# Kernel optimization log

Hardware: AMD Instinct MI355X
Metric: run time of the kernel (lower is better)

## Reference

```python
import jax, jax.numpy as jnp
import numpy as np

Z_DIM, Y_DIM, X_DIM, N_ACT = 32, 16, 64, 4
TINY_H, HEAD_H = 64, 32
INNER_STEPS, SUP_STEPS = 2, 2
BATCH = 524288


def setup_inputs() -> dict:
    key = jax.random.key(0)
    ks = jax.random.split(key, 12)
    s = lambda k, shp, fan_in: jax.random.normal(k, shp, jnp.float32) * (1.0 / np.sqrt(fan_in))
    return {
        "state": jax.random.normal(ks[0], (BATCH, X_DIM), jnp.float32),
        "prev_action": jax.random.randint(ks[1], (BATCH, 1), 0, N_ACT, jnp.int64),
        "z0": jax.random.normal(ks[2], (1, 1, Z_DIM), jnp.float32) * 0.1,
        # TinyNetwork: Linear(112 -> 64), Linear(64 -> 32); weights stored [out, in]
        "Wt1": s(ks[3], (TINY_H, Z_DIM + X_DIM + Y_DIM), Z_DIM + X_DIM + Y_DIM),
        "bt1": jnp.zeros((TINY_H,), jnp.float32),
        "Wt2": s(ks[4], (Z_DIM, TINY_H), TINY_H),
        "bt2": jnp.zeros((Z_DIM,), jnp.float32),
        # OutputHead: Linear(48 -> 32), Linear(32 -> 4)
        "Wh1": s(ks[5], (HEAD_H, Z_DIM + Y_DIM), Z_DIM + Y_DIM),
        "bh1": jnp.zeros((HEAD_H,), jnp.float32),
        "Wh2": s(ks[6], (N_ACT, HEAD_H), HEAD_H),
        "bh2": jnp.zeros((N_ACT,), jnp.float32),
        # action embedding table [n_actions, y_dim]
        "emb": jax.random.normal(ks[7], (N_ACT, Y_DIM), jnp.float32),
    }


def reference(state, prev_action, z0, Wt1, bt1, Wt2, bt2, Wh1, bh1, Wh2, bh2, emb):
    B = state.shape[0]
    x = state[:, None, :]                      # [B, 1, x_dim]
    y = emb[prev_action]                       # [B, 1, y_dim]
    z = jnp.broadcast_to(z0, (B, 1, Z_DIM))    # [B, 1, z_dim]

    def tiny(z, x, y):
        inp = jnp.concatenate([z, x, y], axis=-1)           # [B,1,112]
        h = jax.nn.relu(inp @ Wt1.T + bt1)                  # [B,1,64]
        return h @ Wt2.T + bt2                              # [B,1,32]

    def head(z, y):
        inp = jnp.concatenate([z, y], axis=-1)              # [B,1,48]
        h = jax.nn.relu(inp @ Wh1.T + bh1)                  # [B,1,32]
        return h @ Wh2.T + bh2                              # [B,1,4]

    logits = None
    for _ in range(SUP_STEPS):
        for _ in range(INNER_STEPS):
            z = tiny(z, x, y)
        logits = head(z, y)
        probs = jax.nn.softmax(logits, axis=-1)             # [B,1,4]
        y = probs @ emb                                     # [B,1,16]
    return logits[:, 0, :]                                  # squeeze seq dim
```

## Files before the change

kernel.cpp:

```cpp
#include <hip/hip_runtime.h>
#include <hip/hip_bf16.h>

typedef __attribute__((ext_vector_type(8))) short bf16x8;
typedef __attribute__((ext_vector_type(4))) float f32x4;

#define MFMA16(A,B,C) __builtin_amdgcn_mfma_f32_16x16x32_bf16((A),(B),(C),0,0,0)

static __device__ __forceinline__ f32x4 ld4(const float* p){
  return *(const f32x4*)p;
}
static __device__ __forceinline__ unsigned pk2(float a, float b){
  unsigned r;
  asm("v_cvt_pk_bf16_f32 %0, %1, %2" : "=v"(r) : "v"(a), "v"(b));
  return r;
}
static __device__ __forceinline__ bf16x8 mk8(float a,float b,float c,float d,
                                             float e,float f,float g,float h){
  union { bf16x8 v; unsigned u[4]; } r;
  r.u[0]=pk2(a,b); r.u[1]=pk2(c,d); r.u[2]=pk2(e,f); r.u[3]=pk2(g,h);
  return r.v;
}
static __device__ __forceinline__ bf16x8 mk8v(f32x4 a, f32x4 b){
  return mk8(a[0],a[1],a[2],a[3],b[0],b[1],b[2],b[3]);
}
static __device__ __forceinline__ bf16x8 mk8r(f32x4 a, f32x4 b){
  return mk8(fmaxf(a[0],0.f),fmaxf(a[1],0.f),fmaxf(a[2],0.f),fmaxf(a[3],0.f),
             fmaxf(b[0],0.f),fmaxf(b[1],0.f),fmaxf(b[2],0.f),fmaxf(b[3],0.f));
}
static __device__ __forceinline__ bf16x8 zero8(){
  bf16x8 v;
  #pragma unroll
  for(int i=0;i<8;++i) v[i]=0;
  return v;
}
static __device__ __forceinline__ void keepv(bf16x8& v){ asm("" : "+v"(v)); }
static __device__ __forceinline__ void keepf(f32x4& v){ asm("" : "+v"(v)); }

__global__ __launch_bounds__(256, 1) void trm_mfma(
    const float* __restrict__ state, const int* __restrict__ pact,
    const float* __restrict__ z0,
    const float* __restrict__ Wt1, const float* __restrict__ bt1,
    const float* __restrict__ Wt2, const float* __restrict__ bt2,
    const float* __restrict__ Wh1, const float* __restrict__ bh1,
    const float* __restrict__ Wh2, const float* __restrict__ bh2,
    const float* __restrict__ emb, float* __restrict__ out,
    int ntiles, int wstride)
{
  const int lane = threadIdx.x & 63;
  const int wid  = blockIdx.x * (blockDim.x >> 6) + (threadIdx.x >> 6);
  const int r16  = lane & 15;
  const int hi   = lane >> 4;
  const int he   = hi & 1;

  bf16x8 wt1f[4][4];
  #pragma unroll
  for (int m=0;m<4;++m){
    const float* w = Wt1 + (m*16 + r16)*112;
    wt1f[m][0] = mk8v(ld4(w + hi*4),       ld4(w + 16 + hi*4));
    wt1f[m][1] = mk8v(ld4(w + 32 + hi*8),  ld4(w + 36 + hi*8));
    wt1f[m][2] = mk8v(ld4(w + 64 + hi*8),  ld4(w + 68 + hi*8));
    bf16x8 yfrag = mk8v(ld4(w + 96 + he*8), ld4(w + 100 + he*8));
    if (hi >= 2) yfrag = zero8();
    wt1f[m][3] = yfrag;
    keepv(wt1f[m][0]); keepv(wt1f[m][1]); keepv(wt1f[m][2]); keepv(wt1f[m][3]);
  }
  bf16x8 wt2f[2][2];
  #pragma unroll
  for (int m=0;m<2;++m){
    const float* w = Wt2 + (m*16 + r16)*64;
    wt2f[m][0] = mk8v(ld4(w + hi*4),      ld4(w + 16 + hi*4));
    wt2f[m][1] = mk8v(ld4(w + 32 + hi*4), ld4(w + 48 + hi*4));
    keepv(wt2f[m][0]); keepv(wt2f[m][1]);
  }
  bf16x8 wh1f[2][2];
  #pragma unroll
  for (int m=0;m<2;++m){
    const float* w = Wh1 + (m*16 + r16)*48;
    wh1f[m][0] = mk8v(ld4(w + hi*4), ld4(w + 16 + hi*4));
    bf16x8 yfrag = mk8v(ld4(w + 32 + he*8), ld4(w + 36 + he*8));
    if (hi >= 2) yfrag = zero8();
    wh1f[m][1] = yfrag;
    keepv(wh1f[m][0]); keepv(wh1f[m][1]);
  }
  bf16x8 wh2f;
  {
    const float* w = Wh2 + ((r16 < 4) ? r16 : 0)*32;
    bf16x8 t = mk8v(ld4(w + hi*4), ld4(w + 16 + hi*4));
    if (r16 >= 4) t = zero8();
    wh2f = t;
    keepv(wh2f);
  }
  f32x4 bt1r[4], bt2r[2], bh1r[2], bh2r;
  #pragma unroll
  for (int m=0;m<4;++m){ bt1r[m] = ld4(bt1 + m*16 + hi*4); keepf(bt1r[m]); }
  #pragma unroll
  for (int m=0;m<2;++m){ bt2r[m] = ld4(bt2 + m*16 + hi*4); keepf(bt2r[m]); }
  #pragma unroll
  for (int m=0;m<2;++m){ bh1r[m] = ld4(bh1 + m*16 + hi*4); keepf(bh1r[m]); }
  {
    f32x4 t = ld4(bh2);
    float msk = (hi == 0) ? 1.f : 0.f;
    bh2r = t * msk;
    keepf(bh2r);
  }
  bf16x8 z0f = mk8v(ld4(z0 + hi*4), ld4(z0 + 16 + hi*4));
  keepv(z0f);

  int t = wid;
  f32x4 cx0, cx1, cx2, cx3; int cact;
  {
    const int col = t*16 + r16;
    const float* xr = state + (size_t)col*64;
    cx0 = ld4(xr + hi*8);      cx1 = ld4(xr + hi*8 + 4);
    cx2 = ld4(xr + 32 + hi*8); cx3 = ld4(xr + 36 + hi*8);
    cact = pact[col];
  }

  #pragma unroll 1
  for (; t < ntiles; t += wstride){
    const int tn = t + wstride;
    f32x4 nx0, nx1, nx2, nx3; int nact = 0;
    if (tn < ntiles){
      const int coln = tn*16 + r16;
      const float* xrn = state + (size_t)coln*64;
      nx0 = ld4(xrn + hi*8);      nx1 = ld4(xrn + hi*8 + 4);
      nx2 = ld4(xrn + 32 + hi*8); nx3 = ld4(xrn + 36 + hi*8);
      nact = pact[coln];
    }

    const int col = t*16 + r16;
    bf16x8 xf0 = mk8v(cx0, cx1);
    bf16x8 xf1 = mk8v(cx2, cx3);
    bf16x8 yf;
    {
      const float* er = emb + cact*16 + he*8;
      yf = mk8v(ld4(er), ld4(er + 4));
      if (hi >= 2) yf = zero8();
    }
    bf16x8 zf = z0f;
    f32x4 lgv;

    #pragma unroll
    for (int s=0;s<2;++s){
      #pragma unroll
      for (int it=0; it<2; ++it){
        f32x4 c0=bt1r[0], c1=bt1r[1], c2=bt1r[2], c3=bt1r[3];
        c0=MFMA16(wt1f[0][0], zf,  c0); c1=MFMA16(wt1f[1][0], zf,  c1);
        c2=MFMA16(wt1f[2][0], zf,  c2); c3=MFMA16(wt1f[3][0], zf,  c3);
        c0=MFMA16(wt1f[0][1], xf0, c0); c1=MFMA16(wt1f[1][1], xf0, c1);
        c2=MFMA16(wt1f[2][1], xf0, c2); c3=MFMA16(wt1f[3][1], xf0, c3);
        c0=MFMA16(wt1f[0][2], xf1, c0); c1=MFMA16(wt1f[1][2], xf1, c1);
        c2=MFMA16(wt1f[2][2], xf1, c2); c3=MFMA16(wt1f[3][2], xf1, c3);
        c0=MFMA16(wt1f[0][3], yf,  c0); c1=MFMA16(wt1f[1][3], yf,  c1);
        c2=MFMA16(wt1f[2][3], yf,  c2); c3=MFMA16(wt1f[3][3], yf,  c3);
        bf16x8 h0 = mk8r(c0, c1);
        bf16x8 h1 = mk8r(c2, c3);
        f32x4 d0 = bt2r[0], d1 = bt2r[1];
        d0=MFMA16(wt2f[0][0], h0, d0); d1=MFMA16(wt2f[1][0], h0, d1);
        d0=MFMA16(wt2f[0][1], h1, d0); d1=MFMA16(wt2f[1][1], h1, d1);
        zf = mk8v(d0, d1);
      }
      f32x4 g0 = bh1r[0], g1 = bh1r[1];
      g0=MFMA16(wh1f[0][0], zf, g0); g1=MFMA16(wh1f[1][0], zf, g1);
      g0=MFMA16(wh1f[0][1], yf, g0); g1=MFMA16(wh1f[1][1], yf, g1);
      bf16x8 hh = mk8r(g0, g1);
      f32x4 cl = bh2r;
      cl = MFMA16(wh2f, hh, cl);
      lgv = cl;
      if (s == 0){
        float l0 = __shfl(cl[0], r16), l1 = __shfl(cl[1], r16);
        float l2 = __shfl(cl[2], r16), l3 = __shfl(cl[3], r16);
        float mx = fmaxf(fmaxf(l0,l1), fmaxf(l2,l3));
        float p0=__expf(l0-mx), p1=__expf(l1-mx);
        float p2=__expf(l2-mx), p3=__expf(l3-mx);
        float inv = 1.f/(p0+p1+p2+p3);
        p0*=inv; p1*=inv; p2*=inv; p3*=inv;
        const float* eb = emb + he*8;
        f32x4 ya = ld4(eb)*p0      + ld4(eb+16)*p1 +
                   ld4(eb+32)*p2   + ld4(eb+48)*p3;
        f32x4 yb = ld4(eb+4)*p0    + ld4(eb+20)*p1 +
                   ld4(eb+36)*p2   + ld4(eb+52)*p3;
        yf = mk8v(ya, yb);
        if (hi >= 2) yf = zero8();
      }
    }
    if (hi == 0) *(f32x4*)(out + (size_t)col*4) = lgv;

    cx0 = nx0; cx1 = nx1; cx2 = nx2; cx3 = nx3; cact = nact;
  }
}

extern "C" void kernel_launch(void* const* d_in, const int* in_sizes, int n_in,
                              void* d_out, int out_size, void* d_ws, size_t ws_size,
                              hipStream_t stream) {
  const float* state = (const float*)d_in[0];
  const int*   pact  = (const int*)  d_in[1];
  const float* z0    = (const float*)d_in[2];
  const float* Wt1   = (const float*)d_in[3];
  const float* bt1   = (const float*)d_in[4];
  const float* Wt2   = (const float*)d_in[5];
  const float* bt2   = (const float*)d_in[6];
  const float* Wh1   = (const float*)d_in[7];
  const float* bh1   = (const float*)d_in[8];
  const float* Wh2   = (const float*)d_in[9];
  const float* bh2   = (const float*)d_in[10];
  const float* emb   = (const float*)d_in[11];
  float* out = (float*)d_out;

  const int B = in_sizes[0] / 64;
  const int ntiles = B / 16;
  const int blocks = 1024;
  const int wstride = blocks * 4;
  trm_mfma<<<blocks, 256, 0, stream>>>(state, pact, z0, Wt1, bt1, Wt2, bt2,
                                       Wh1, bh1, Wh2, bh2, emb, out,
                                       ntiles, wstride);
}
```

Baseline: 69.50 us.

## Process two 16-row tiles per wave iteration to interleave independent MFMA chains

```diff
diff --git a/kernel.cpp b/kernel.cpp
--- a/kernel.cpp
+++ b/kernel.cpp
@@ -44,7 +44,7 @@
     const float* __restrict__ Wh1, const float* __restrict__ bh1,
     const float* __restrict__ Wh2, const float* __restrict__ bh2,
     const float* __restrict__ emb, float* __restrict__ out,
-    int ntiles, int wstride)
+    int niters, int wstride)
 {
   const int lane = threadIdx.x & 63;
   const int wid  = blockIdx.x * (blockDim.x >> 6) + (threadIdx.x >> 6);
@@ -106,87 +106,133 @@
   bf16x8 z0f = mk8v(ld4(z0 + hi*4), ld4(z0 + 16 + hi*4));
   keepv(z0f);
 
-  int t = wid;
-  f32x4 cx0, cx1, cx2, cx3; int cact;
+  int it = wid;
+  f32x4 ax0, ax1, ax2, ax3, bx0, bx1, bx2, bx3;
+  int aact, bact;
   {
-    const int col = t*16 + r16;
-    const float* xr = state + (size_t)col*64;
-    cx0 = ld4(xr + hi*8);      cx1 = ld4(xr + hi*8 + 4);
-    cx2 = ld4(xr + 32 + hi*8); cx3 = ld4(xr + 36 + hi*8);
-    cact = pact[col];
+    const int colA = it*32 + r16, colB = colA + 16;
+    const float* xa = state + (size_t)colA*64;
+    const float* xb = state + (size_t)colB*64;
+    ax0 = ld4(xa + hi*8);      ax1 = ld4(xa + hi*8 + 4);
+    ax2 = ld4(xa + 32 + hi*8); ax3 = ld4(xa + 36 + hi*8);
+    bx0 = ld4(xb + hi*8);      bx1 = ld4(xb + hi*8 + 4);
+    bx2 = ld4(xb + 32 + hi*8); bx3 = ld4(xb + 36 + hi*8);
+    aact = pact[colA]; bact = pact[colB];
   }
 
   #pragma unroll 1
-  for (; t < ntiles; t += wstride){
-    const int tn = t + wstride;
-    f32x4 nx0, nx1, nx2, nx3; int nact = 0;
-    if (tn < ntiles){
-      const int coln = tn*16 + r16;
-      const float* xrn = state + (size_t)coln*64;
-      nx0 = ld4(xrn + hi*8);      nx1 = ld4(xrn + hi*8 + 4);
-      nx2 = ld4(xrn + 32 + hi*8); nx3 = ld4(xrn + 36 + hi*8);
-      nact = pact[coln];
-    }
-
-    const int col = t*16 + r16;
-    bf16x8 xf0 = mk8v(cx0, cx1);
-    bf16x8 xf1 = mk8v(cx2, cx3);
-    bf16x8 yf;
+  for (; it < niters; it += wstride){
+    const int colA = it*32 + r16, colB = colA + 16;
+
+    bf16x8 xfA0 = mk8v(ax0, ax1), xfA1 = mk8v(ax2, ax3);
+    bf16x8 xfB0 = mk8v(bx0, bx1), xfB1 = mk8v(bx2, bx3);
+    bf16x8 yfA, yfB;
     {
-      const float* er = emb + cact*16 + he*8;
-      yf = mk8v(ld4(er), ld4(er + 4));
-      if (hi >= 2) yf = zero8();
-    }
-    bf16x8 zf = z0f;
-    f32x4 lgv;
+      const float* er = emb + aact*16 + he*8;
+      yfA = mk8v(ld4(er), ld4(er + 4));
+      if (hi >= 2) yfA = zero8();
+    }
+    {
+      const float* er = emb + bact*16 + he*8;
+      yfB = mk8v(ld4(er), ld4(er + 4));
+      if (hi >= 2) yfB = zero8();
+    }
+
+    const int itn = it + wstride;
+    if (itn < niters){
+      const int cAn = itn*32 + r16, cBn = cAn + 16;
+      const float* xa = state + (size_t)cAn*64;
+      const float* xb = state + (size_t)cBn*64;
+      ax0 = ld4(xa + hi*8);      ax1 = ld4(xa + hi*8 + 4);
+      ax2 = ld4(xa + 32 + hi*8); ax3 = ld4(xa + 36 + hi*8);
+      bx0 = ld4(xb + hi*8);      bx1 = ld4(xb + hi*8 + 4);
+      bx2 = ld4(xb + 32 + hi*8); bx3 = ld4(xb + 36 + hi*8);
+      aact = pact[cAn]; bact = pact[cBn];
+    }
+
+    bf16x8 zfA = z0f, zfB = z0f;
+    f32x4 lgvA, lgvB;
 
     #pragma unroll
-    for (int s=0;s<2;++s){
+    for (int s = 0; s < 2; ++s){
       #pragma unroll
-      for (int it=0; it<2; ++it){
-        f32x4 c0=bt1r[0], c1=bt1r[1], c2=bt1r[2], c3=bt1r[3];
-        c0=MFMA16(wt1f[0][0], zf,  c0); c1=MFMA16(wt1f[1][0], zf,  c1);
-        c2=MFMA16(wt1f[2][0], zf,  c2); c3=MFMA16(wt1f[3][0], zf,  c3);
-        c0=MFMA16(wt1f[0][1], xf0, c0); c1=MFMA16(wt1f[1][1], xf0, c1);
-        c2=MFMA16(wt1f[2][1], xf0, c2); c3=MFMA16(wt1f[3][1], xf0, c3);
-        c0=MFMA16(wt1f[0][2], xf1, c0); c1=MFMA16(wt1f[1][2], xf1, c1);
-        c2=MFMA16(wt1f[2][2], xf1, c2); c3=MFMA16(wt1f[3][2], xf1, c3);
-        c0=MFMA16(wt1f[0][3], yf,  c0); c1=MFMA16(wt1f[1][3], yf,  c1);
-        c2=MFMA16(wt1f[2][3], yf,  c2); c3=MFMA16(wt1f[3][3], yf,  c3);
-        bf16x8 h0 = mk8r(c0, c1);
-        bf16x8 h1 = mk8r(c2, c3);
-        f32x4 d0 = bt2r[0], d1 = bt2r[1];
-        d0=MFMA16(wt2f[0][0], h0, d0); d1=MFMA16(wt2f[1][0], h0, d1);
-        d0=MFMA16(wt2f[0][1], h1, d0); d1=MFMA16(wt2f[1][1], h1, d1);
-        zf = mk8v(d0, d1);
+      for (int itr = 0; itr < 2; ++itr){
+        f32x4 cA0=bt1r[0], cA1=bt1r[1], cA2=bt1r[2], cA3=bt1r[3];
+        f32x4 cB0=bt1r[0], cB1=bt1r[1], cB2=bt1r[2], cB3=bt1r[3];
+        cA0=MFMA16(wt1f[0][0],zfA,cA0);  cB0=MFMA16(wt1f[0][0],zfB,cB0);
+        cA1=MFMA16(wt1f[1][0],zfA,cA1);  cB1=MFMA16(wt1f[1][0],zfB,cB1);
+        cA2=MFMA16(wt1f[2][0],zfA,cA2);  cB2=MFMA16(wt1f[2][0],zfB,cB2);
+        cA3=MFMA16(wt1f[3][0],zfA,cA3);  cB3=MFMA16(wt1f[3][0],zfB,cB3);
+        cA0=MFMA16(wt1f[0][1],xfA0,cA0); cB0=MFMA16(wt1f[0][1],xfB0,cB0);
+        cA1=MFMA16(wt1f[1][1],xfA0,cA1); cB1=MFMA16(wt1f[1][1],xfB0,cB1);
+        cA2=MFMA16(wt1f[2][1],xfA0,cA2); cB2=MFMA16(wt1f[2][1],xfB0,cB2);
+        cA3=MFMA16(wt1f[3][1],xfA0,cA3); cB3=MFMA16(wt1f[3][1],xfB0,cB3);
+        cA0=MFMA16(wt1f[0][2],xfA1,cA0); cB0=MFMA16(wt1f[0][2],xfB1,cB0);
+        cA1=MFMA16(wt1f[1][2],xfA1,cA1); cB1=MFMA16(wt1f[1][2],xfB1,cB1);
+        cA2=MFMA16(wt1f[2][2],xfA1,cA2); cB2=MFMA16(wt1f[2][2],xfB1,cB2);
+        cA3=MFMA16(wt1f[3][2],xfA1,cA3); cB3=MFMA16(wt1f[3][2],xfB1,cB3);
+        cA0=MFMA16(wt1f[0][3],yfA,cA0);  cB0=MFMA16(wt1f[0][3],yfB,cB0);
+        cA1=MFMA16(wt1f[1][3],yfA,cA1);  cB1=MFMA16(wt1f[1][3],yfB,cB1);
+        cA2=MFMA16(wt1f[2][3],yfA,cA2);  cB2=MFMA16(wt1f[2][3],yfB,cB2);
+        cA3=MFMA16(wt1f[3][3],yfA,cA3);  cB3=MFMA16(wt1f[3][3],yfB,cB3);
+        bf16x8 hA0 = mk8r(cA0, cA1), hA1 = mk8r(cA2, cA3);
+        bf16x8 hB0 = mk8r(cB0, cB1), hB1 = mk8r(cB2, cB3);
+        f32x4 dA0=bt2r[0], dA1=bt2r[1], dB0=bt2r[0], dB1=bt2r[1];
+        dA0=MFMA16(wt2f[0][0],hA0,dA0); dB0=MFMA16(wt2f[0][0],hB0,dB0);
+        dA1=MFMA16(wt2f[1][0],hA0,dA1); dB1=MFMA16(wt2f[1][0],hB0,dB1);
+        dA0=MFMA16(wt2f[0][1],hA1,dA0); dB0=MFMA16(wt2f[0][1],hB1,dB0);
+        dA1=MFMA16(wt2f[1][1],hA1,dA1); dB1=MFMA16(wt2f[1][1],hB1,dB1);
+        zfA = mk8v(dA0, dA1); zfB = mk8v(dB0, dB1);
       }
-      f32x4 g0 = bh1r[0], g1 = bh1r[1];
-      g0=MFMA16(wh1f[0][0], zf, g0); g1=MFMA16(wh1f[1][0], zf, g1);
-      g0=MFMA16(wh1f[0][1], yf, g0); g1=MFMA16(wh1f[1][1], yf, g1);
-      bf16x8 hh = mk8r(g0, g1);
-      f32x4 cl = bh2r;
-      cl = MFMA16(wh2f, hh, cl);
-      lgv = cl;
+      f32x4 gA0=bh1r[0], gA1=bh1r[1], gB0=bh1r[0], gB1=bh1r[1];
+      gA0=MFMA16(wh1f[0][0],zfA,gA0); gB0=MFMA16(wh1f[0][0],zfB,gB0);
+      gA1=MFMA16(wh1f[1][0],zfA,gA1); gB1=MFMA16(wh1f[1][0],zfB,gB1);
+      gA0=MFMA16(wh1f[0][1],yfA,gA0); gB0=MFMA16(wh1f[0][1],yfB,gB0);
+      gA1=MFMA16(wh1f[1][1],yfA,gA1); gB1=MFMA16(wh1f[1][1],yfB,gB1);
+      bf16x8 hhA = mk8r(gA0, gA1), hhB = mk8r(gB0, gB1);
+      f32x4 clA = bh2r, clB = bh2r;
+      clA = MFMA16(wh2f, hhA, clA);
+      clB = MFMA16(wh2f, hhB, clB);
+      lgvA = clA; lgvB = clB;
       if (s == 0){
-        float l0 = __shfl(cl[0], r16), l1 = __shfl(cl[1], r16);
-        float l2 = __shfl(cl[2], r16), l3 = __shfl(cl[3], r16);
-        float mx = fmaxf(fmaxf(l0,l1), fmaxf(l2,l3));
-        float p0=__expf(l0-mx), p1=__expf(l1-mx);
-        float p2=__expf(l2-mx), p3=__expf(l3-mx);
-        float inv = 1.f/(p0+p1+p2+p3);
-        p0*=inv; p1*=inv; p2*=inv; p3*=inv;
-        const float* eb = emb + he*8;
-        f32x4 ya = ld4(eb)*p0      + ld4(eb+16)*p1 +
-                   ld4(eb+32)*p2   + ld4(eb+48)*p3;
-        f32x4 yb = ld4(eb+4)*p0    + ld4(eb+20)*p1 +
-                   ld4(eb+36)*p2   + ld4(eb+52)*p3;
-        yf = mk8v(ya, yb);
-        if (hi >= 2) yf = zero8();
+        {
+          float l0=__shfl(clA[0],r16), l1=__shfl(clA[1],r16);
+          float l2=__shfl(clA[2],r16), l3=__shfl(clA[3],r16);
+          float mx = fmaxf(fmaxf(l0,l1), fmaxf(l2,l3));
+          float p0=__expf(l0-mx), p1=__expf(l1-mx);
+          float p2=__expf(l2-mx), p3=__expf(l3-mx);
+          float inv = 1.f/(p0+p1+p2+p3);
+          p0*=inv; p1*=inv; p2*=inv; p3*=inv;
+          const float* eb = emb + he*8;
+          f32x4 ya = ld4(eb)*p0    + ld4(eb+16)*p1 +
+                     ld4(eb+32)*p2 + ld4(eb+48)*p3;
+          f32x4 yb = ld4(eb+4)*p0  + ld4(eb+20)*p1 +
+                     ld4(eb+36)*p2 + ld4(eb+52)*p3;
+          yfA = mk8v(ya, yb);
+          if (hi >= 2) yfA = zero8();
+        }
+        {
+          float l0=__shfl(clB[0],r16), l1=__shfl(clB[1],r16);
+          float l2=__shfl(clB[2],r16), l3=__shfl(clB[3],r16);
+          float mx = fmaxf(fmaxf(l0,l1), fmaxf(l2,l3));
+          float p0=__expf(l0-mx), p1=__expf(l1-mx);
+          float p2=__expf(l2-mx), p3=__expf(l3-mx);
+          float inv = 1.f/(p0+p1+p2+p3);
+          p0*=inv; p1*=inv; p2*=inv; p3*=inv;
+          const float* eb = emb + he*8;
+          f32x4 ya = ld4(eb)*p0    + ld4(eb+16)*p1 +
+                     ld4(eb+32)*p2 + ld4(eb+48)*p3;
+          f32x4 yb = ld4(eb+4)*p0  + ld4(eb+20)*p1 +
+                     ld4(eb+36)*p2 + ld4(eb+52)*p3;
+          yfB = mk8v(ya, yb);
+          if (hi >= 2) yfB = zero8();
+        }
       }
     }
-    if (hi == 0) *(f32x4*)(out + (size_t)col*4) = lgv;
-
-    cx0 = nx0; cx1 = nx1; cx2 = nx2; cx3 = nx3; cact = nact;
+    if (hi == 0){
+      *(f32x4*)(out + (size_t)colA*4) = lgvA;
+      *(f32x4*)(out + (size_t)colB*4) = lgvB;
+    }
   }
 }
 
@@ -208,10 +254,10 @@
   float* out = (float*)d_out;
 
   const int B = in_sizes[0] / 64;
-  const int ntiles = B / 16;
+  const int niters = B / 32;
   const int blocks = 1024;
   const int wstride = blocks * 4;
   trm_mfma<<<blocks, 256, 0, stream>>>(state, pact, z0, Wt1, bt1, Wt2, bt2,
                                        Wh1, bh1, Wh2, bh2, emb, out,
-                                       ntiles, wstride);
-}
+                                       niters, wstride);
+}
```

Result: slower. 72.02 us (+3.6%).
